# Optimization experiments

Hardware: AMD Instinct MI355X
Metric: run time of the kernel (lower is better)

## Reference

```python
import jax, jax.numpy as jnp
import numpy as np

N_NODES = 50000
N_EDGES = 800000
F_IN = 128
HID = 64
N_LAYERS = 3
N_GRAPHS = 64
N_CLASS = 2


def setup_inputs() -> dict:
    key = jax.random.key(0)
    ks = jax.random.split(key, 8)
    x = jax.random.normal(ks[0], (N_NODES, F_IN), jnp.float32)
    edge_index = jax.random.randint(ks[1], (2, N_EDGES), 0, N_NODES, dtype=jnp.int32)
    # sorted, balanced graph assignment so every graph id appears (max-pool safe)
    batch = (jnp.arange(N_NODES, dtype=jnp.int32) * N_GRAPHS) // N_NODES

    def lin(k, fi, fo):
        return jax.random.normal(k, (fi, fo), jnp.float32) / np.sqrt(fi).astype(np.float32)

    W1 = lin(ks[2], F_IN, HID)
    W2 = lin(ks[3], HID, HID)
    W3 = lin(ks[4], HID, HID)
    lin1_W = lin(ks[5], 3 * N_LAYERS * HID, HID)
    lin2_W = lin(ks[6], HID, N_CLASS)
    return dict(
        x=x,
        W1=W1, b1=jnp.zeros((HID,), jnp.float32),
        W2=W2, b2=jnp.zeros((HID,), jnp.float32),
        W3=W3, b3=jnp.zeros((HID,), jnp.float32),
        lin1_W=lin1_W, lin1_b=jnp.zeros((HID,), jnp.float32),
        lin2_W=lin2_W, lin2_b=jnp.zeros((N_CLASS,), jnp.float32),
        edge_index=edge_index, batch=batch,
    )


def reference(x, W1, b1, W2, b2, W3, b3, lin1_W, lin1_b, lin2_W, lin2_b,
              edge_index, batch):
    src, dst = edge_index[0], edge_index[1]
    # GCN symmetric normalization with self-loops (computed once, shared by layers)
    deg = jax.ops.segment_sum(jnp.ones((N_EDGES,), jnp.float32), dst, N_NODES) + 1.0
    dinv = jax.lax.rsqrt(deg)                      # [N]
    enorm = dinv[src] * dinv[dst]                  # [E]
    self_norm = (dinv * dinv)[:, None]             # [N,1] self-loop coeff

    def gcn_conv(h, W, b):
        h = h @ W                                  # [N, HID]
        agg = jax.ops.segment_sum(h[src] * enorm[:, None], dst, N_NODES)
        return agg + self_norm * h + b

    h = jax.nn.relu(gcn_conv(x, W1, b1))
    xs = [h]
    for W, b in ((W2, b2), (W3, b3)):
        h = jax.nn.relu(gcn_conv(h, W, b))
        xs.append(h)
    hcat = jnp.concatenate(xs, axis=1)             # JK 'cat': [N, 3*HID]

    add = jax.ops.segment_sum(hcat, batch, N_GRAPHS)
    cnt = jax.ops.segment_sum(jnp.ones((N_NODES,), jnp.float32), batch, N_GRAPHS)
    mean = add / cnt[:, None]
    mx = jax.ops.segment_max(hcat, batch, N_GRAPHS)
    g = jnp.concatenate([add, mean, mx], axis=1)   # [G, 9*HID]

    g = jax.nn.relu(g @ lin1_W + lin1_b)
    # dropout p=0.5 is identity in eval mode
    logits = g @ lin2_W + lin2_b
    return jax.nn.log_softmax(logits, axis=-1)
```

## Files before the change

kernel.cpp:

```cpp
#include <hip/hip_runtime.h>
#include <hip/hip_fp16.h>

#define N_NODES 50000
#define N_EDGES 800000
#define F_IN 128
#define HID 64
#define N_GRAPHS 64

#define SCAN_B ((N_NODES + 255) / 256)
#define FUSE_B ((N_EDGES + 255) / 256)

typedef _Float16 half8 __attribute__((ext_vector_type(8)));
typedef float f32x4 __attribute__((ext_vector_type(4)));

__global__ void deg_pack(const int* __restrict__ ei, int* __restrict__ ideg, int E,
                         const float* __restrict__ W1, const float* __restrict__ W2,
                         const float* __restrict__ W3,
                         __half* __restrict__ W1t, __half* __restrict__ W2t,
                         __half* __restrict__ W3t) {
    int i = blockIdx.x * blockDim.x + threadIdx.x;
    if (i * 4 < E) {
        int4 d = ((const int4*)(ei + E))[i];
        atomicAdd(&ideg[d.x], 1);
        atomicAdd(&ideg[d.y], 1);
        atomicAdd(&ideg[d.z], 1);
        atomicAdd(&ideg[d.w], 1);
    }
    if (i < 8192) {
        int f = i >> 7, k = i & 127;
        W1t[i] = __float2half(W1[k * 64 + f]);
    } else if (i < 12288) {
        int j = i - 8192;
        int f = j >> 6, k = j & 63;
        W2t[j] = __float2half(W2[k * 64 + f]);
    } else if (i < 16384) {
        int l = i - 12288;
        int f = l >> 6, k = l & 63;
        W3t[l] = __float2half(W3[k * 64 + f]);
    }
}

__global__ void scan_part(const int* __restrict__ ideg, int* __restrict__ bsum,
                          float* __restrict__ padd, unsigned int* __restrict__ pmax,
                          int* __restrict__ pcnt, int n) {
    __shared__ int s[256];
    int t = threadIdx.x;
    if (blockIdx.x < 48) {
        int z = blockIdx.x * 256 + t;
        padd[z] = 0.f;
        pmax[z] = 0u;
        if (z < 64) pcnt[z] = 0;
    }
    int i = blockIdx.x * 256 + t;
    s[t] = (i < n) ? ideg[i] : 0;
    __syncthreads();
    for (int o = 128; o > 0; o >>= 1) {
        if (t < o) s[t] += s[t + o];
        __syncthreads();
    }
    if (t == 0) bsum[blockIdx.x] = s[0];
}

__global__ void scan_final(const int* __restrict__ ideg, const int* __restrict__ bsum,
                           int* __restrict__ offs, int* __restrict__ cur,
                           float* __restrict__ dinv, int n) {
    __shared__ int s[256];
    __shared__ int sb[256];
    int t = threadIdx.x;
    int i = blockIdx.x * 256 + t;
    int v = (i < n) ? ideg[i] : 0;
    s[t] = v;
    sb[t] = (t < SCAN_B) ? bsum[t] : 0;
    __syncthreads();
    for (int o = 1; o < 256; o <<= 1) {
        int u  = (t >= o) ? s[t - o] : 0;
        int ub = (t >= o) ? sb[t - o] : 0;
        __syncthreads();
        s[t] += u; sb[t] += ub;
        __syncthreads();
    }
    int base = (blockIdx.x == 0) ? 0 : sb[blockIdx.x - 1];
    int excl = base + s[t] - v;
    if (i < n) {
        offs[i] = excl; cur[i] = excl;
        dinv[i] = rsqrtf((float)v + 1.0f);
    }
    if (i == n - 1) offs[n] = excl + v;
}

__global__ __launch_bounds__(256) void fused_fill_mm1(
        const int* __restrict__ ei, const float* __restrict__ dinv,
        int* __restrict__ cur, unsigned short* __restrict__ csr,
        const float* __restrict__ X, const __half* __restrict__ W1t,
        __half* __restrict__ Y16, int E) {
    constexpr int SX = 136;
    __shared__ __half sXh[16 * SX];
    int tid = threadIdx.x;

    int e = blockIdx.x * 256 + tid;
    unsigned short srcu = (unsigned short)(ei[e] & 0xFFFF);
    int d = ei[E + e];
    int pos = atomicAdd(&cur[d], 1);

    int lane = tid & 63;
    int r = lane & 15, h = lane >> 4;
    int w = tid >> 6;
    const half8* Brow = (const half8*)(W1t + (size_t)(w * 16 + r) * F_IN + h * 8);
    half8 b0 = Brow[0];
    half8 b1 = Brow[4];
    half8 b2 = Brow[8];
    half8 b3 = Brow[12];

    int nodeBase = blockIdx.x * 16;
#pragma unroll
    for (int p = tid; p < 512; p += 256) {
        int row = p >> 5, c4 = p & 31;
        float4 v = *(const float4*)(X + (size_t)(nodeBase + row) * F_IN + c4 * 4);
        __half2 ab = __floats2half2_rn(v.x, v.y);
        __half2 cd = __floats2half2_rn(v.z, v.w);
        uint2 u; u.x = *(unsigned int*)&ab; u.y = *(unsigned int*)&cd;
        *(uint2*)&sXh[row * SX + c4 * 4] = u;
    }
    __syncthreads();

    f32x4 acc = {0.f, 0.f, 0.f, 0.f};
    half8 a0 = *(const half8*)&sXh[r * SX +  0 + h * 8];
    half8 a1 = *(const half8*)&sXh[r * SX + 32 + h * 8];
    half8 a2 = *(const half8*)&sXh[r * SX + 64 + h * 8];
    half8 a3 = *(const half8*)&sXh[r * SX + 96 + h * 8];
    acc = __builtin_amdgcn_mfma_f32_16x16x32_f16(a0, b0, acc, 0, 0, 0);
    acc = __builtin_amdgcn_mfma_f32_16x16x32_f16(a1, b1, acc, 0, 0, 0);
    acc = __builtin_amdgcn_mfma_f32_16x16x32_f16(a2, b2, acc, 0, 0, 0);
    acc = __builtin_amdgcn_mfma_f32_16x16x32_f16(a3, b3, acc, 0, 0, 0);
    int nodeT = nodeBase + h * 4;
    float4 dv = *(const float4*)(dinv + nodeT);
    acc[0] *= dv.x; acc[1] *= dv.y; acc[2] *= dv.z; acc[3] *= dv.w;
#pragma unroll
    for (int reg = 0; reg < 4; ++reg)
        Y16[(size_t)(nodeT + reg) * 64 + w * 16 + r] = __float2half(acc[reg]);

    csr[pos] = srcu;
}

__global__ __launch_bounds__(256) void matmul64_h(
        const __half* __restrict__ X, const __half* __restrict__ Wt,
        const float* __restrict__ dinv, __half* __restrict__ Y16, int n) {
    int tid = threadIdx.x;
    int nodeBase = blockIdx.x * 64;
    int lane = tid & 63;
    int r = lane & 15, h = lane >> 4;
    int w = tid >> 6;
    int rowA = nodeBase + w * 16 + r;
    const half8* Arow = (const half8*)(X + (size_t)rowA * 64 + h * 8);
    half8 a0 = Arow[0];
    half8 a1 = Arow[4];
    int nodeT = nodeBase + w * 16 + h * 4;
    float4 dv = *(const float4*)(dinv + nodeT);
#pragma unroll
    for (int ft = 0; ft < 4; ++ft) {
        const half8* Brow = (const half8*)(Wt + (size_t)(ft * 16 + r) * 64 + h * 8);
        half8 b0 = Brow[0];
        half8 b1 = Brow[4];
        f32x4 acc = {0.f, 0.f, 0.f, 0.f};
        acc = __builtin_amdgcn_mfma_f32_16x16x32_f16(a0, b0, acc, 0, 0, 0);
        acc = __builtin_amdgcn_mfma_f32_16x16x32_f16(a1, b1, acc, 0, 0, 0);
        acc[0] *= dv.x; acc[1] *= dv.y; acc[2] *= dv.z; acc[3] *= dv.w;
#pragma unroll
        for (int reg = 0; reg < 4; ++reg) {
            int node = nodeT + reg;
            if (node < n) Y16[(size_t)node * 64 + ft * 16 + r] = __float2half(acc[reg]);
        }
    }
}

__global__ void agg_kernel(const __half* __restrict__ hp16, const float* __restrict__ dinv,
                           const int* __restrict__ offs, const unsigned short* __restrict__ csr,
                           const float* __restrict__ b, __half* __restrict__ hout, int n) {
    int node = blockIdx.x * 4 + (threadIdx.x >> 6);
    if (node >= n) return;
    int lane = threadIdx.x & 63;
    int g = lane >> 3;
    int sub = lane & 7;
    int beg = offs[node], end = offs[node + 1];

    float dn = dinv[node];
    uint4 sv = *(const uint4*)(hp16 + (size_t)node * 64 + sub * 8);
    float4 bA = *(const float4*)(b + sub * 8);
    float4 bB = *(const float4*)(b + sub * 8 + 4);

    float a0 = 0.f, a1 = 0.f, a2 = 0.f, a3 = 0.f;
    float a4 = 0.f, a5 = 0.f, a6 = 0.f, a7 = 0.f;
    int lim = end - 1;
#pragma unroll 1
    for (int base0 = beg; base0 < end; base0 += 32) {
        int base = base0 + g * 4;
        if (base < end) {
            int i0 = base, i1 = min(base + 1, lim), i2 = min(base + 2, lim), i3 = min(base + 3, lim);
            unsigned short s0 = csr[i0], s1 = csr[i1], s2 = csr[i2], s3 = csr[i3];
            uint4 hv0 = *(const uint4*)(hp16 + (size_t)s0 * 64 + sub * 8);
            uint4 hv1 = *(const uint4*)(hp16 + (size_t)s1 * 64 + sub * 8);
            uint4 hv2 = *(const uint4*)(hp16 + (size_t)s2 * 64 + sub * 8);
            uint4 hv3 = *(const uint4*)(hp16 + (size_t)s3 * 64 + sub * 8);
#pragma unroll
            for (int j = 0; j < 4; ++j) {
                uint4 hvj = (j == 0) ? hv0 : (j == 1) ? hv1 : (j == 2) ? hv2 : hv3;
                float w = (base + j < end) ? 1.f : 0.f;
                float2 f01 = __half22float2(*(const __half2*)&hvj.x);
                float2 f23 = __half22float2(*(const __half2*)&hvj.y);
                float2 f45 = __half22float2(*(const __half2*)&hvj.z);
                float2 f67 = __half22float2(*(const __half2*)&hvj.w);
                a0 += f01.x * w; a1 += f01.y * w; a2 += f23.x * w; a3 += f23.y * w;
                a4 += f45.x * w; a5 += f45.y * w; a6 += f67.x * w; a7 += f67.y * w;
            }
        }
    }
#pragma unroll
    for (int m = 8; m <= 32; m <<= 1) {
        a0 += __shfl_xor(a0, m); a1 += __shfl_xor(a1, m);
        a2 += __shfl_xor(a2, m); a3 += __shfl_xor(a3, m);
        a4 += __shfl_xor(a4, m); a5 += __shfl_xor(a5, m);
        a6 += __shfl_xor(a6, m); a7 += __shfl_xor(a7, m);
    }

    float2 s01 = __half22float2(*(const __half2*)&sv.x);
    float2 s23 = __half22float2(*(const __half2*)&sv.y);
    float2 s45 = __half22float2(*(const __half2*)&sv.z);
    float2 s67 = __half22float2(*(const __half2*)&sv.w);
    float4 rA, rB;
    rA.x = dn * (a0 + s01.x) + bA.x;  rA.x = rA.x > 0.f ? rA.x : 0.f;
    rA.y = dn * (a1 + s01.y) + bA.y;  rA.y = rA.y > 0.f ? rA.y : 0.f;
    rA.z = dn * (a2 + s23.x) + bA.z;  rA.z = rA.z > 0.f ? rA.z : 0.f;
    rA.w = dn * (a3 + s23.y) + bA.w;  rA.w = rA.w > 0.f ? rA.w : 0.f;
    rB.x = dn * (a4 + s45.x) + bB.x;  rB.x = rB.x > 0.f ? rB.x : 0.f;
    rB.y = dn * (a5 + s45.y) + bB.y;  rB.y = rB.y > 0.f ? rB.y : 0.f;
    rB.z = dn * (a6 + s67.x) + bB.z;  rB.z = rB.z > 0.f ? rB.z : 0.f;
    rB.w = dn * (a7 + s67.y) + bB.w;  rB.w = rB.w > 0.f ? rB.w : 0.f;
    if (g == 0) {
        __half2 p0 = __floats2half2_rn(rA.x, rA.y);
        __half2 p1 = __floats2half2_rn(rA.z, rA.w);
        __half2 p2 = __floats2half2_rn(rB.x, rB.y);
        __half2 p3 = __floats2half2_rn(rB.z, rB.w);
        uint4 st;
        st.x = *(unsigned int*)&p0; st.y = *(unsigned int*)&p1;
        st.z = *(unsigned int*)&p2; st.w = *(unsigned int*)&p3;
        *(uint4*)(hout + (size_t)node * 64 + sub * 8) = st;
    }
}

__global__ __launch_bounds__(192) void pool_kernel(
        const __half* __restrict__ h1, const __half* __restrict__ h2,
        const __half* __restrict__ h3, const int* __restrict__ batch,
        float* __restrict__ padd, unsigned int* __restrict__ pmax,
        int* __restrict__ pcnt, int n, int chunk) {
    __shared__ float lsum[8][192];
    __shared__ float lmax[8][192];
    int t = threadIdx.x;
    int stream = t / 24;
    int oct = t % 24;
    int L = oct >> 3, sub = oct & 7;
    int f0 = L * 64 + sub * 8;
    const __half* src = (L == 0) ? h1 : (L == 1) ? h2 : h3;
    int start = blockIdx.x * chunk;
    int end = min(start + chunk, n);
    if (start >= end) return;
    int gtail = batch[end - 1];

    float s[8] = {0.f,0.f,0.f,0.f,0.f,0.f,0.f,0.f};
    float m[8] = {0.f,0.f,0.f,0.f,0.f,0.f,0.f,0.f};
    int cnt = 0;
    int node = start + stream;
    int gcur = (node < end) ? batch[node] : gtail;
    for (; node < end; node += 8) {
        int bg = batch[node];
        if (bg != gcur) {
#pragma unroll
            for (int j = 0; j < 8; ++j) {
                unsafeAtomicAdd(&padd[gcur * 192 + f0 + j], s[j]);
                atomicMax(&pmax[gcur * 192 + f0 + j], __float_as_uint(m[j]));
                s[j] = 0.f; m[j] = 0.f;
            }
            if (oct == 0) { atomicAdd(&pcnt[gcur], cnt); cnt = 0; }
            gcur = bg;
        }
        uint4 hv = *(const uint4*)(src + (size_t)node * 64 + sub * 8);
        const __half2* hp = (const __half2*)&hv;
#pragma unroll
        for (int q = 0; q < 4; ++q) {
            float2 f2 = __half22float2(hp[q]);
            s[2*q]   += f2.x;  m[2*q]   = fmaxf(m[2*q],   f2.x);
            s[2*q+1] += f2.y;  m[2*q+1] = fmaxf(m[2*q+1], f2.y);
        }
        if (oct == 0) ++cnt;
    }
    if (oct == 0 && cnt) atomicAdd(&pcnt[gcur], cnt);
    if (gcur != gtail) {
#pragma unroll
        for (int j = 0; j < 8; ++j) {
            unsafeAtomicAdd(&padd[gcur * 192 + f0 + j], s[j]);
            atomicMax(&pmax[gcur * 192 + f0 + j], __float_as_uint(m[j]));
            s[j] = 0.f; m[j] = 0.f;
        }
    }
#pragma unroll
    for (int j = 0; j < 8; ++j) {
        lsum[stream][f0 + j] = s[j];
        lmax[stream][f0 + j] = m[j];
    }
    __syncthreads();
    float ts = 0.f, tm = 0.f;
#pragma unroll
    for (int st = 0; st < 8; ++st) {
        ts += lsum[st][t];
        tm = fmaxf(tm, lmax[st][t]);
    }
    unsafeAtomicAdd(&padd[gtail * 192 + t], ts);
    atomicMax(&pmax[gtail * 192 + t], __float_as_uint(tm));
}

__global__ void mlp_kernel(const float* __restrict__ padd, const unsigned int* __restrict__ pmax,
                           const int* __restrict__ pcnt,
                           const float* __restrict__ lin1_W, const float* __restrict__ lin1_b,
                           const float* __restrict__ lin2_W, const float* __restrict__ lin2_b,
                           float* __restrict__ out) {
    int g = blockIdx.x;
    int t = threadIdx.x;
    __shared__ float gv[576];
    __shared__ float hid[64];
    float cnt = (float)pcnt[g];
    for (int i = t; i < 192; i += 64) {
        float a = padd[g * 192 + i];
        gv[i] = a;
        gv[192 + i] = a / cnt;
        gv[384 + i] = __uint_as_float(pmax[g * 192 + i]);
    }
    __syncthreads();
    float acc = lin1_b[t];
#pragma unroll 8
    for (int k = 0; k < 576; ++k) acc += gv[k] * lin1_W[k * 64 + t];
    hid[t] = acc > 0.0f ? acc : 0.0f;
    __syncthreads();
    if (t == 0) {
        float l0 = lin2_b[0], l1 = lin2_b[1];
        for (int k = 0; k < 64; ++k) {
            l0 += hid[k] * lin2_W[k * 2 + 0];
            l1 += hid[k] * lin2_W[k * 2 + 1];
        }
        float m = fmaxf(l0, l1);
        float lse = m + logf(expf(l0 - m) + expf(l1 - m));
        out[g * 2 + 0] = l0 - lse;
        out[g * 2 + 1] = l1 - lse;
    }
}

extern "C" void kernel_launch(void* const* d_in, const int* in_sizes, int n_in,
                              void* d_out, int out_size, void* d_ws, size_t ws_size,
                              hipStream_t stream) {
    const float* x      = (const float*)d_in[0];
    const float* W1     = (const float*)d_in[1];
    const float* b1     = (const float*)d_in[2];
    const float* W2     = (const float*)d_in[3];
    const float* b2     = (const float*)d_in[4];
    const float* W3     = (const float*)d_in[5];
    const float* b3     = (const float*)d_in[6];
    const float* lin1_W = (const float*)d_in[7];
    const float* lin1_b = (const float*)d_in[8];
    const float* lin2_W = (const float*)d_in[9];
    const float* lin2_b = (const float*)d_in[10];
    const int*   ei     = (const int*)d_in[11];
    const int*   batch  = (const int*)d_in[12];
    float* out = (float*)d_out;

    char* ws = (char*)d_ws;
    size_t off = 0;
    auto alloc = [&](size_t bytes) {
        void* p = ws + off;
        off = (off + bytes + 255) & ~(size_t)255;
        return p;
    };
    int*   ideg    = (int*)  alloc(N_NODES * 4);
    float* dinv    = (float*)alloc(N_NODES * 4);
    int*   offs    = (int*)  alloc((N_NODES + 1) * 4);
    int*   cur     = (int*)  alloc(N_NODES * 4);
    int*   bsum    = (int*)  alloc(SCAN_B * 4);
    unsigned short* csr = (unsigned short*)alloc((size_t)N_EDGES * 2);
    __half* P      = (__half*)alloc((size_t)N_NODES * 64 * 2);
    __half* h1     = (__half*)alloc((size_t)N_NODES * 64 * 2);
    __half* h2     = (__half*)alloc((size_t)N_NODES * 64 * 2);
    __half* h3     = (__half*)alloc((size_t)N_NODES * 64 * 2);
    __half* W1t    = (__half*)alloc(64 * 128 * 2);
    __half* W2t    = (__half*)alloc(64 * 64 * 2);
    __half* W3t    = (__half*)alloc(64 * 64 * 2);
    float* padd    = (float*)alloc(N_GRAPHS * 192 * 4);
    unsigned int* pmax = (unsigned int*)alloc(N_GRAPHS * 192 * 4);
    int*   pcnt    = (int*) alloc(N_GRAPHS * 4);

    hipMemsetAsync(ideg, 0, N_NODES * 4, stream);
    deg_pack<<<(N_EDGES / 4 + 255) / 256, 256, 0, stream>>>(ei, ideg, N_EDGES,
                                                            W1, W2, W3, W1t, W2t, W3t);
    scan_part <<<SCAN_B, 256, 0, stream>>>(ideg, bsum, padd, pmax, pcnt, N_NODES);
    scan_final<<<SCAN_B, 256, 0, stream>>>(ideg, bsum, offs, cur, dinv, N_NODES);

    const int mmGrid  = (N_NODES + 63) / 64;
    const int aggGrid = (N_NODES + 3) / 4;

    fused_fill_mm1<<<FUSE_B, 256, 0, stream>>>(ei, dinv, cur, csr, x, W1t, P, N_EDGES);
    agg_kernel<<<aggGrid, 256, 0, stream>>>(P, dinv, offs, csr, b1, h1, N_NODES);
    matmul64_h<<<mmGrid, 256, 0, stream>>>(h1, W2t, dinv, P, N_NODES);
    agg_kernel<<<aggGrid, 256, 0, stream>>>(P, dinv, offs, csr, b2, h2, N_NODES);
    matmul64_h<<<mmGrid, 256, 0, stream>>>(h2, W3t, dinv, P, N_NODES);
    agg_kernel<<<aggGrid, 256, 0, stream>>>(P, dinv, offs, csr, b3, h3, N_NODES);

    const int chunk = (N_NODES + 511) / 512;
    pool_kernel<<<512, 192, 0, stream>>>(h1, h2, h3, batch, padd, pmax, pcnt, N_NODES, chunk);
    mlp_kernel<<<N_GRAPHS, 64, 0, stream>>>(padd, pmax, pcnt, lin1_W, lin1_b, lin2_W, lin2_b, out);
}
```

Before: 319.9 us.

## Record edge rank during degree count to drop second atomic CSR fill pass

The degree-counting kernel now keeps the return value of each atomicAdd as the edge's rank within its destination bucket and stores it as a 16-bit value. The CSR fill then computes each position as offs[d] + rank[e] instead of issuing a second round of 800k atomics on a cursor array, and the cursor array is removed. Per-graph node counts also move from atomics in the pool kernel to a shared-memory histogram in the scan kernel. In exchange there is an extra 1.6 MB rank write and read, and the rank is truncated to 16 bits, which limits it to in-degrees below 65536.

```diff
diff --git a/kernel.cpp b/kernel.cpp
--- a/kernel.cpp
+++ b/kernel.cpp
@@ -13,7 +13,8 @@
 typedef _Float16 half8 __attribute__((ext_vector_type(8)));
 typedef float f32x4 __attribute__((ext_vector_type(4)));
 
-__global__ void deg_pack(const int* __restrict__ ei, int* __restrict__ ideg, int E,
+__global__ void deg_pack(const int* __restrict__ ei, int* __restrict__ ideg,
+                         unsigned short* __restrict__ rank, int* __restrict__ pcnt, int E,
                          const float* __restrict__ W1, const float* __restrict__ W2,
                          const float* __restrict__ W3,
                          __half* __restrict__ W1t, __half* __restrict__ W2t,
@@ -21,11 +22,14 @@
     int i = blockIdx.x * blockDim.x + threadIdx.x;
     if (i * 4 < E) {
         int4 d = ((const int4*)(ei + E))[i];
-        atomicAdd(&ideg[d.x], 1);
-        atomicAdd(&ideg[d.y], 1);
-        atomicAdd(&ideg[d.z], 1);
-        atomicAdd(&ideg[d.w], 1);
-    }
+        unsigned short r0 = (unsigned short)atomicAdd(&ideg[d.x], 1);
+        unsigned short r1 = (unsigned short)atomicAdd(&ideg[d.y], 1);
+        unsigned short r2 = (unsigned short)atomicAdd(&ideg[d.z], 1);
+        unsigned short r3 = (unsigned short)atomicAdd(&ideg[d.w], 1);
+        ushort4 rr; rr.x = r0; rr.y = r1; rr.z = r2; rr.w = r3;
+        *(ushort4*)(rank + i * 4) = rr;
+    }
+    if (i < 64) pcnt[i] = 0;
     if (i < 8192) {
         int f = i >> 7, k = i & 127;
         W1t[i] = __float2half(W1[k * 64 + f]);
@@ -41,29 +45,32 @@
 }
 
 __global__ void scan_part(const int* __restrict__ ideg, int* __restrict__ bsum,
+                          const int* __restrict__ batch,
                           float* __restrict__ padd, unsigned int* __restrict__ pmax,
                           int* __restrict__ pcnt, int n) {
     __shared__ int s[256];
+    __shared__ int hcnt[N_GRAPHS];
     int t = threadIdx.x;
     if (blockIdx.x < 48) {
         int z = blockIdx.x * 256 + t;
         padd[z] = 0.f;
         pmax[z] = 0u;
-        if (z < 64) pcnt[z] = 0;
-    }
+    }
+    if (t < N_GRAPHS) hcnt[t] = 0;
     int i = blockIdx.x * 256 + t;
     s[t] = (i < n) ? ideg[i] : 0;
     __syncthreads();
+    if (i < n) atomicAdd(&hcnt[batch[i]], 1);
     for (int o = 128; o > 0; o >>= 1) {
         if (t < o) s[t] += s[t + o];
         __syncthreads();
     }
     if (t == 0) bsum[blockIdx.x] = s[0];
+    if (t < N_GRAPHS && hcnt[t]) atomicAdd(&pcnt[t], hcnt[t]);
 }
 
 __global__ void scan_final(const int* __restrict__ ideg, const int* __restrict__ bsum,
-                           int* __restrict__ offs, int* __restrict__ cur,
-                           float* __restrict__ dinv, int n) {
+                           int* __restrict__ offs, float* __restrict__ dinv, int n) {
     __shared__ int s[256];
     __shared__ int sb[256];
     int t = threadIdx.x;
@@ -82,7 +89,7 @@
     int base = (blockIdx.x == 0) ? 0 : sb[blockIdx.x - 1];
     int excl = base + s[t] - v;
     if (i < n) {
-        offs[i] = excl; cur[i] = excl;
+        offs[i] = excl;
         dinv[i] = rsqrtf((float)v + 1.0f);
     }
     if (i == n - 1) offs[n] = excl + v;
@@ -90,7 +97,8 @@
 
 __global__ __launch_bounds__(256) void fused_fill_mm1(
         const int* __restrict__ ei, const float* __restrict__ dinv,
-        int* __restrict__ cur, unsigned short* __restrict__ csr,
+        const int* __restrict__ offs, const unsigned short* __restrict__ rank,
+        unsigned short* __restrict__ csr,
         const float* __restrict__ X, const __half* __restrict__ W1t,
         __half* __restrict__ Y16, int E) {
     constexpr int SX = 136;
@@ -100,7 +108,7 @@
     int e = blockIdx.x * 256 + tid;
     unsigned short srcu = (unsigned short)(ei[e] & 0xFFFF);
     int d = ei[E + e];
-    int pos = atomicAdd(&cur[d], 1);
+    int pos = offs[d] + (int)rank[e];
 
     int lane = tid & 63;
     int r = lane & 15, h = lane >> 4;
@@ -250,8 +258,7 @@
 __global__ __launch_bounds__(192) void pool_kernel(
         const __half* __restrict__ h1, const __half* __restrict__ h2,
         const __half* __restrict__ h3, const int* __restrict__ batch,
-        float* __restrict__ padd, unsigned int* __restrict__ pmax,
-        int* __restrict__ pcnt, int n, int chunk) {
+        float* __restrict__ padd, unsigned int* __restrict__ pmax, int n, int chunk) {
     __shared__ float lsum[8][192];
     __shared__ float lmax[8][192];
     int t = threadIdx.x;
@@ -267,7 +274,6 @@
 
     float s[8] = {0.f,0.f,0.f,0.f,0.f,0.f,0.f,0.f};
     float m[8] = {0.f,0.f,0.f,0.f,0.f,0.f,0.f,0.f};
-    int cnt = 0;
     int node = start + stream;
     int gcur = (node < end) ? batch[node] : gtail;
     for (; node < end; node += 8) {
@@ -279,7 +285,6 @@
                 atomicMax(&pmax[gcur * 192 + f0 + j], __float_as_uint(m[j]));
                 s[j] = 0.f; m[j] = 0.f;
             }
-            if (oct == 0) { atomicAdd(&pcnt[gcur], cnt); cnt = 0; }
             gcur = bg;
         }
         uint4 hv = *(const uint4*)(src + (size_t)node * 64 + sub * 8);
@@ -290,9 +295,7 @@
             s[2*q]   += f2.x;  m[2*q]   = fmaxf(m[2*q],   f2.x);
             s[2*q+1] += f2.y;  m[2*q+1] = fmaxf(m[2*q+1], f2.y);
         }
-        if (oct == 0) ++cnt;
-    }
-    if (oct == 0 && cnt) atomicAdd(&pcnt[gcur], cnt);
+    }
     if (gcur != gtail) {
 #pragma unroll
         for (int j = 0; j < 8; ++j) {
@@ -380,9 +383,9 @@
     int*   ideg    = (int*)  alloc(N_NODES * 4);
     float* dinv    = (float*)alloc(N_NODES * 4);
     int*   offs    = (int*)  alloc((N_NODES + 1) * 4);
-    int*   cur     = (int*)  alloc(N_NODES * 4);
     int*   bsum    = (int*)  alloc(SCAN_B * 4);
-    unsigned short* csr = (unsigned short*)alloc((size_t)N_EDGES * 2);
+    unsigned short* rank = (unsigned short*)alloc((size_t)N_EDGES * 2);
+    unsigned short* csr  = (unsigned short*)alloc((size_t)N_EDGES * 2);
     __half* P      = (__half*)alloc((size_t)N_NODES * 64 * 2);
     __half* h1     = (__half*)alloc((size_t)N_NODES * 64 * 2);
     __half* h2     = (__half*)alloc((size_t)N_NODES * 64 * 2);
@@ -395,15 +398,15 @@
     int*   pcnt    = (int*) alloc(N_GRAPHS * 4);
 
     hipMemsetAsync(ideg, 0, N_NODES * 4, stream);
-    deg_pack<<<(N_EDGES / 4 + 255) / 256, 256, 0, stream>>>(ei, ideg, N_EDGES,
+    deg_pack<<<(N_EDGES / 4 + 255) / 256, 256, 0, stream>>>(ei, ideg, rank, pcnt, N_EDGES,
                                                             W1, W2, W3, W1t, W2t, W3t);
-    scan_part <<<SCAN_B, 256, 0, stream>>>(ideg, bsum, padd, pmax, pcnt, N_NODES);
-    scan_final<<<SCAN_B, 256, 0, stream>>>(ideg, bsum, offs, cur, dinv, N_NODES);
+    scan_part <<<SCAN_B, 256, 0, stream>>>(ideg, bsum, batch, padd, pmax, pcnt, N_NODES);
+    scan_final<<<SCAN_B, 256, 0, stream>>>(ideg, bsum, offs, dinv, N_NODES);
 
     const int mmGrid  = (N_NODES + 63) / 64;
     const int aggGrid = (N_NODES + 3) / 4;
 
-    fused_fill_mm1<<<FUSE_B, 256, 0, stream>>>(ei, dinv, cur, csr, x, W1t, P, N_EDGES);
+    fused_fill_mm1<<<FUSE_B, 256, 0, stream>>>(ei, dinv, offs, rank, csr, x, W1t, P, N_EDGES);
     agg_kernel<<<aggGrid, 256, 0, stream>>>(P, dinv, offs, csr, b1, h1, N_NODES);
     matmul64_h<<<mmGrid, 256, 0, stream>>>(h1, W2t, dinv, P, N_NODES);
     agg_kernel<<<aggGrid, 256, 0, stream>>>(P, dinv, offs, csr, b2, h2, N_NODES);
@@ -411,6 +414,6 @@
     agg_kernel<<<aggGrid, 256, 0, stream>>>(P, dinv, offs, csr, b3, h3, N_NODES);
 
     const int chunk = (N_NODES + 511) / 512;
-    pool_kernel<<<512, 192, 0, stream>>>(h1, h2, h3, batch, padd, pmax, pcnt, N_NODES, chunk);
+    pool_kernel<<<512, 192, 0, stream>>>(h1, h2, h3, batch, padd, pmax, N_NODES, chunk);
     mlp_kernel<<<N_GRAPHS, 64, 0, stream>>>(padd, pmax, pcnt, lin1_W, lin1_b, lin2_W, lin2_b, out);
 }
```

After: 281.0 us. 1.14x faster.
